# Kernel tuning notes

Measured on AMD Instinct MI355X. Metric: run time of the kernel, lower is better.

## Reference

```python
import jax, jax.numpy as jnp
import numpy as np

B, L, D, N_HEADS = 4, 8192, 1024, 16
HD = D // N_HEADS
MASK_NEG = -1e10


def setup_inputs() -> dict:
    key = jax.random.key(0)
    ks = jax.random.split(key, 5)
    # xavier_normal std for square Dense: sqrt(2/(fan_in+fan_out))
    std = (2.0 / (D + D)) ** 0.5
    return {
        "query": jax.random.normal(ks[0], (B, L, D), dtype=jnp.float32),
        "mask": jax.random.bernoulli(ks[1], 0.1, (B, L)),  # True = masked out
        "Wq": std * jax.random.normal(ks[2], (D, D), dtype=jnp.float32),
        "bq": jnp.zeros((D,), dtype=jnp.float32),
        "Wk": std * jax.random.normal(ks[3], (D, D), dtype=jnp.float32),
        "bk": jnp.zeros((D,), dtype=jnp.float32),
        "Wv": std * jax.random.normal(ks[4], (D, D), dtype=jnp.float32),
        "bv": jnp.zeros((D,), dtype=jnp.float32),
    }


def reference(query, mask, Wq, bq, Wk, bk, Wv, bv):
    # Self-attention: key = value = query (original falls back when key/value are None)
    q = query @ Wq + bq  # [B, L, D]
    k = query @ Wk + bk
    v = query @ Wv + bv
    # split heads: b l (n h) -> b l n h
    qs = q.reshape(B, L, N_HEADS, HD)
    ks_ = k.reshape(B, L, N_HEADS, HD)
    vs = v.reshape(B, L, N_HEADS, HD)
    m = mask[:, :, None, None]  # [B, L, 1, 1], broadcast over heads & dims
    K = jnp.where(m, MASK_NEG, ks_)
    V = jnp.where(m, 0.0, vs)
    # elu kernel feature map: phi(x) = elu(x) + 1 (elu(-1e10)+1 -> 0 for masked keys)
    phiK = jax.nn.elu(K) + 1.0
    phiQ = jax.nn.elu(qs) + 1.0
    # per-head kv summary: [B, N, HD_k, HD_v]
    kv = jnp.einsum('blnk,blnv->bnkv', phiK, V)
    # FAITHFUL to original einsum 'blk,bkv->blk': sums kv over v, elementwise with phiQ
    kv_sum = kv.sum(-1)  # [B, N, HD]
    out = phiQ * kv_sum[:, None, :, :]  # [B, L, N, HD]
    # combine heads: b l n h -> b l (n h)
    return out.reshape(B, L, D)
```

## Files before the change

kernel.cpp:

```cpp
#include <hip/hip_runtime.h>

typedef unsigned short u16;
typedef unsigned int u32;
typedef __attribute__((ext_vector_type(8))) short s16x8;
typedef __attribute__((ext_vector_type(4))) float f32x4;

#define GAS __attribute__((address_space(1)))
#define LAS __attribute__((address_space(3)))

#define BB 4
#define LL 8192
#define DD 1024
#define NH 16
#define HD 64
#define MROWS (BB * LL)
#define NWBT 2064

__device__ __forceinline__ u16 f2bf(float f) {
  u32 u = __builtin_bit_cast(u32, f);
  u32 r = (u + 0x7FFFu + ((u >> 16) & 1u)) >> 16;
  return (u16)r;
}
__device__ __forceinline__ float bf2f(u32 lo) {
  return __builtin_bit_cast(float, lo << 16);
}

__device__ __forceinline__ void async16(const void* g, void* l) {
  __builtin_amdgcn_global_load_lds((const GAS u32*)g, (LAS u32*)l, 16, 0, 0);
}

__device__ __forceinline__ bool get_mask(const void* mp, int row, int mode) {
  if (mode == 2) return ((const unsigned char*)mp)[row] != 0;
  if (mode == 1) return ((const float*)mp)[row] != 0.f;
  return ((const int*)mp)[row] != 0;
}

__global__ void build_wbt(const float* __restrict__ Wq, const float* __restrict__ Wk,
                          u16* __restrict__ WbT) {
  __shared__ float t[32][33];
  const int n0 = blockIdx.x * 32;
  const int k0 = blockIdx.y * 32;
  const float* W = (n0 >> 10) == 0 ? Wq : Wk;
  const int nloc = n0 & 1023;
  const int tx = threadIdx.x, ty = threadIdx.y;
#pragma unroll
  for (int j = 0; j < 32; j += 8)
    t[ty + j][tx] = W[(size_t)(k0 + ty + j) * DD + nloc + tx];
  __syncthreads();
#pragma unroll
  for (int j = 0; j < 32; j += 8)
    WbT[(size_t)(n0 + ty + j) * DD + k0 + tx] = f2bf(t[tx][ty + j]);
}

__global__ void build_aux(const float* __restrict__ Wv, const float* __restrict__ bq,
                          const float* __restrict__ bk, const float* __restrict__ bv,
                          const u32* __restrict__ m,
                          u16* __restrict__ WbT, float* __restrict__ bcat,
                          int* __restrict__ flag) {
  const int blk = blockIdx.x;
  const int tid = threadIdx.x;
  if (blk < 64) {
    int i = blk * 256 + tid;
    int k = i >> 4, h = i & 15;
    float s = 0.f;
    const float* p = Wv + (size_t)k * DD + h * HD;
#pragma unroll 8
    for (int j = 0; j < 64; ++j) s += p[j];
    WbT[(size_t)(2048 + h) * DD + k] = f2bf(s);
  } else if (blk < 73) {
    int i = (blk - 64) * 256 + tid;
    if (i < 1024) bcat[i] = bq[i];
    else if (i < 2048) bcat[i] = bk[i - 1024];
    else if (i < 2064) {
      float s = 0.f;
      const float* p = bv + (i - 2048) * HD;
#pragma unroll 8
      for (int j = 0; j < 64; ++j) s += p[j];
      bcat[i] = s;
    }
  } else {
    int i = (blk - 73) * 256 + tid;
    u32 v = m[i];
    int f = 0;
    if (v == 0x3F800000u) f = 1;
    else if (v > 1u) f = 2;
    if (f) atomicMax(flag, f);
  }
}

__global__ __launch_bounds__(256) void prep_q(
    const float* __restrict__ query, const u16* __restrict__ WbT,
    const float* __restrict__ bcat, const void* __restrict__ maskp,
    const int* __restrict__ mmode,
    u16* __restrict__ qb, float* __restrict__ sV) {
  __shared__ u16 ldsW[16 * 1024];
  __shared__ u16 ldsA[64 * 64];
  const int tid = threadIdx.x;
  const int lane = tid & 63;
  const int w = tid >> 6;
  const int l15 = lane & 15, l16 = lane >> 4;
  const int row0 = blockIdx.x * 64;

#pragma unroll
  for (int j = 0; j < 8; ++j) {
    int idx = tid + j * 256;
    int h = idx >> 7, c = idx & 127;
    s16x8 v = *(const s16x8*)(WbT + (size_t)(2048 + h) * DD + c * 8);
    *(s16x8*)(ldsW + h * 1024 + (c ^ (h & 7)) * 8) = v;
  }

  f32x4 acc = {};
  for (int k0 = 0; k0 < DD; k0 += 64) {
    __syncthreads();
#pragma unroll
    for (int j = 0; j < 2; ++j) {
      int li = tid + j * 256;
      int row = li >> 3, slot = li & 7;
      int seg = slot ^ (row & 7);
      const float* gp = query + (size_t)(row0 + row) * DD + k0 + seg * 8;
      float4 v0 = *(const float4*)gp;
      float4 v1 = *(const float4*)(gp + 4);
      s16x8 o;
      o[0] = (short)f2bf(v0.x); o[1] = (short)f2bf(v0.y);
      o[2] = (short)f2bf(v0.z); o[3] = (short)f2bf(v0.w);
      o[4] = (short)f2bf(v1.x); o[5] = (short)f2bf(v1.y);
      o[6] = (short)f2bf(v1.z); o[7] = (short)f2bf(v1.w);
      *(s16x8*)(qb + (size_t)(row0 + row) * DD + k0 + seg * 8) = o;
      *(s16x8*)(ldsA + row * 64 + slot * 8) = o;
    }
    __syncthreads();
#pragma unroll
    for (int kk = 0; kk < 2; ++kk) {
      const int segk = kk * 4 + l16;
      const int r = w * 16 + l15;
      s16x8 af = *(const s16x8*)(ldsA + r * 64 + ((segk ^ (r & 7))) * 8);
      const int cc = (k0 >> 3) + segk;
      s16x8 bfr = *(const s16x8*)(ldsW + l15 * 1024 + ((cc ^ (l15 & 7))) * 8);
      acc = __builtin_amdgcn_mfma_f32_16x16x32_bf16(af, bfr, acc, 0, 0, 0);
    }
  }

  const int mode = *mmode;
#pragma unroll
  for (int r = 0; r < 4; ++r) {
    const int row = row0 + w * 16 + l16 * 4 + r;
    const bool msk = get_mask(maskp, row, mode);
    float v = acc[r] + bcat[2048 + l15];
    sV[(size_t)row * NH + l15] = msk ? 0.f : v;
  }
}

#define BUFSZ 8192
#define UOFF(buf, mat, ks) (((((buf)*2 + (mat))*2 + (ks))) * BUFSZ)

__global__ __launch_bounds__(512, 2) void gemm_qkv(
    const u16* __restrict__ qb, const u16* __restrict__ WbT,
    const float* __restrict__ bcat, const void* __restrict__ maskp,
    const int* __restrict__ mmode,
    const float* __restrict__ sV, float* __restrict__ kv,
    float* __restrict__ out, int phase) {
  __shared__ __align__(16) u16 lds[65536];
  const int tid = threadIdx.x;
  const int lane = tid & 63;
  const int w = tid >> 6;
  const int wm = w & 1, wn = w >> 1;
  const int l15 = lane & 15, l16 = lane >> 4;

  const int bid = blockIdx.x;
  const int swz = (bid & 7) * 64 + (bid >> 3);
  const int mt = swz >> 2;
  const int nt = swz & 3;
  const int row0 = mt * 256;
  const int col0 = (phase ? 1024 : 0) + nt * 256;

  f32x4 acc[8][4] = {};

#define STAGE(buf, mat, ks, kt) do {                                        \
    const u16* gb_ = (mat) ? (WbT + (size_t)col0 * DD)                      \
                           : (qb + (size_t)row0 * DD);                      \
    const int kt_ = (kt) & 15;                                              \
    _Pragma("unroll")                                                       \
    for (int j_ = 0; j_ < 2; ++j_) {                                        \
      int li_ = tid + j_ * 512;                                             \
      int row_ = li_ >> 2, slot_ = li_ & 3;                                 \
      int c_ = slot_ ^ ((row_ >> 1) & 3);                                   \
      async16(gb_ + (size_t)row_ * DD + kt_ * 64 + (ks) * 32 + c_ * 8,      \
              lds + UOFF(buf, mat, ks) + li_ * 8);                          \
    }                                                                       \
  } while (0)

#define LDA(buf, ks, a) do {                                                \
    _Pragma("unroll")                                                       \
    for (int mi_ = 0; mi_ < 8; ++mi_) {                                     \
      int r_ = wm * 128 + mi_ * 16 + l15;                                   \
      a[mi_] = *(const s16x8*)(lds + UOFF(buf, 0, ks) + r_ * 32 +           \
                               ((l16 ^ ((r_ >> 1) & 3)) * 8));              \
    }                                                                       \
  } while (0)

#define LDB2(buf, ks, nb, b) do {                                           \
    _Pragma("unroll")                                                       \
    for (int q_ = 0; q_ < 2; ++q_) {                                        \
      int r_ = wn * 64 + ((nb)*2 + q_) * 16 + l15;                          \
      b[q_] = *(const s16x8*)(lds + UOFF(buf, 1, ks) + r_ * 32 +            \
                              ((l16 ^ ((r_ >> 1) & 3)) * 8));               \
    }                                                                       \
  } while (0)

#define MM(a, b, nb) do {                                                   \
    __builtin_amdgcn_s_setprio(1);                                          \
    _Pragma("unroll")                                                       \
    for (int mi_ = 0; mi_ < 8; ++mi_) {                                     \
      acc[mi_][(nb)*2] = __builtin_amdgcn_mfma_f32_16x16x32_bf16(           \
          a[mi_], b[0], acc[mi_][(nb)*2], 0, 0, 0);                         \
      acc[mi_][(nb)*2 + 1] = __builtin_amdgcn_mfma_f32_16x16x32_bf16(       \
          a[mi_], b[1], acc[mi_][(nb)*2 + 1], 0, 0, 0);                     \
    }                                                                       \
    __builtin_amdgcn_s_setprio(0);                                          \
  } while (0)

#define BAR() __builtin_amdgcn_s_barrier()
#define VMW6() asm volatile("s_waitcnt vmcnt(6)" ::: "memory")

  STAGE(0, 0, 0, 0); STAGE(0, 1, 0, 0); STAGE(0, 0, 1, 0); STAGE(0, 1, 1, 0);
  STAGE(1, 0, 0, 1); STAGE(1, 1, 0, 1); STAGE(1, 0, 1, 1);
  VMW6();
  BAR();

  for (int t = 0; t < 16; t += 2) {
    s16x8 a[8], b[2];
    LDA(0, 0, a); LDB2(0, 0, 0, b);
    STAGE(1, 1, 1, t + 1);
    BAR(); MM(a, b, 0); BAR();
    LDB2(0, 0, 1, b);
    STAGE(0, 0, 0, t + 2);
    BAR(); MM(a, b, 1); BAR();
    LDA(0, 1, a); LDB2(0, 1, 0, b);
    STAGE(0, 1, 0, t + 2);
    BAR(); MM(a, b, 0); BAR();
    LDB2(0, 1, 1, b);
    STAGE(0, 0, 1, t + 2);
    BAR(); MM(a, b, 1); VMW6(); BAR();
    LDA(1, 0, a); LDB2(1, 0, 0, b);
    STAGE(0, 1, 1, t + 2);
    BAR(); MM(a, b, 0); BAR();
    LDB2(1, 0, 1, b);
    STAGE(1, 0, 0, t + 3);
    BAR(); MM(a, b, 1); BAR();
    LDA(1, 1, a); LDB2(1, 1, 0, b);
    STAGE(1, 1, 0, t + 3);
    BAR(); MM(a, b, 0); BAR();
    LDB2(1, 1, 1, b);
    STAGE(1, 0, 1, t + 3);
    BAR(); MM(a, b, 1); VMW6(); BAR();
  }

  const int mode = *mmode;
  const int lanec = lane & 15, laneq = lane >> 4;
  const int wcol0 = col0 + wn * 64;
  const int b_ = row0 >> 13;

  if (phase == 1) {
    const int n = (wcol0 - 1024) >> 6;
    float pc[4] = {0.f, 0.f, 0.f, 0.f};
#pragma unroll
    for (int mi = 0; mi < 8; ++mi) {
#pragma unroll
      for (int r = 0; r < 4; ++r) {
        const int row = row0 + wm * 128 + mi * 16 + laneq * 4 + r;
        const bool msk = get_mask(maskp, row, mode);
        if (!msk) {
          const float sv = sV[(size_t)row * NH + n];
#pragma unroll
          for (int ni = 0; ni < 4; ++ni) {
            const int col = wcol0 + ni * 16 + lanec;
            float v = acc[mi][ni][r] + bcat[col];
            float phi = v > 0.f ? v + 1.f : __expf(v);
            pc[ni] += phi * sv;
          }
        }
      }
    }
#pragma unroll
    for (int ni = 0; ni < 4; ++ni) {
      pc[ni] += __shfl_xor(pc[ni], 16);
      pc[ni] += __shfl_xor(pc[ni], 32);
    }
    if (laneq == 0) {
#pragma unroll
      for (int ni = 0; ni < 4; ++ni) {
        const int colk = wcol0 - 1024 + ni * 16 + lanec;
        atomicAdd(&kv[b_ * DD + colk], pc[ni]);
      }
    }
  } else {
    float kvv[4];
#pragma unroll
    for (int ni = 0; ni < 4; ++ni)
      kvv[ni] = kv[b_ * DD + wcol0 + ni * 16 + lanec];
#pragma unroll
    for (int mi = 0; mi < 8; ++mi) {
#pragma unroll
      for (int r = 0; r < 4; ++r) {
        const int row = row0 + wm * 128 + mi * 16 + laneq * 4 + r;
#pragma unroll
        for (int ni = 0; ni < 4; ++ni) {
          const int col = wcol0 + ni * 16 + lanec;
          float v = acc[mi][ni][r] + bcat[col];
          float phi = v > 0.f ? v + 1.f : __expf(v);
          out[(size_t)row * DD + col] = phi * kvv[ni];
        }
      }
    }
  }
}

extern "C" void kernel_launch(void* const* d_in, const int* in_sizes, int n_in,
                              void* d_out, int out_size, void* d_ws, size_t ws_size,
                              hipStream_t stream) {
  const float* query = (const float*)d_in[0];
  const void* maskp = d_in[1];
  const float* Wq = (const float*)d_in[2];
  const float* bq = (const float*)d_in[3];
  const float* Wk = (const float*)d_in[4];
  const float* bk = (const float*)d_in[5];
  const float* Wv = (const float*)d_in[6];
  const float* bv = (const float*)d_in[7];
  float* out = (float*)d_out;

  char* ws = (char*)d_ws;
  u16* qb = (u16*)ws;            ws += (size_t)MROWS * DD * 2;
  u16* WbT = (u16*)ws;           ws += (size_t)NWBT * DD * 2;
  float* sV = (float*)ws;        ws += (size_t)MROWS * NH * 4;
  float* bcat = (float*)ws;      ws += (size_t)NWBT * 4;
  float* kv = (float*)ws;        ws += (size_t)BB * DD * 4;
  int* mflag = (int*)ws;         ws += 256;

  hipMemsetAsync(kv, 0, (size_t)BB * DD * 4 + 256, stream);

  build_wbt<<<dim3(2048 / 32, DD / 32), dim3(32, 8), 0, stream>>>(Wq, Wk, WbT);
  build_aux<<<105, 256, 0, stream>>>(Wv, bq, bk, bv, (const u32*)maskp, WbT, bcat, mflag);
  prep_q<<<MROWS / 64, 256, 0, stream>>>(query, WbT, bcat, maskp, mflag, qb, sV);
  gemm_qkv<<<512, 512, 0, stream>>>(qb, WbT, bcat, maskp, mflag, sV, kv, out, 1);
  gemm_qkv<<<512, 512, 0, stream>>>(qb, WbT, bcat, maskp, mflag, sV, kv, out, 0);
}
```

Before: 418.2 us.

## Load prep_q operands straight into registers and split K across wave pairs

The prep_q kernel no longer stages the 16-row WbT slice and the query tile through LDS with per-iteration barriers. Each wave now loads fp32 query rows and weight fragments directly into registers in MFMA fragment layout, converts them to bf16, stores the bf16 copy, and issues MFMAs. The K dimension is split between two waves whose partial sums are combined through a small shared buffer, and the grid doubles to 32 rows per block. This removes the LDS staging and the synchronisation overhead, at the cost of higher register pressure and redundant global loads of the weight slice across waves.

```diff
diff --git a/kernel.cpp b/kernel.cpp
--- a/kernel.cpp
+++ b/kernel.cpp
@@ -93,60 +93,58 @@
     const float* __restrict__ bcat, const void* __restrict__ maskp,
     const int* __restrict__ mmode,
     u16* __restrict__ qb, float* __restrict__ sV) {
-  __shared__ u16 ldsW[16 * 1024];
-  __shared__ u16 ldsA[64 * 64];
+  __shared__ float sVp[2][16][16];
   const int tid = threadIdx.x;
   const int lane = tid & 63;
   const int w = tid >> 6;
+  const int wl = w >> 1;
+  const int ks = w & 1;
   const int l15 = lane & 15, l16 = lane >> 4;
-  const int row0 = blockIdx.x * 64;
-
-#pragma unroll
-  for (int j = 0; j < 8; ++j) {
-    int idx = tid + j * 256;
-    int h = idx >> 7, c = idx & 127;
-    s16x8 v = *(const s16x8*)(WbT + (size_t)(2048 + h) * DD + c * 8);
-    *(s16x8*)(ldsW + h * 1024 + (c ^ (h & 7)) * 8) = v;
-  }
+  const int row0 = blockIdx.x * 32 + wl * 16;
+  const int arow = row0 + l15;
+
+  const float* qrow = query + (size_t)arow * DD + ks * 512 + l16 * 8;
+  u16* qbrow = qb + (size_t)arow * DD + ks * 512 + l16 * 8;
+  const u16* wrow = WbT + (size_t)(2048 + l15) * DD + ks * 512 + l16 * 8;
 
   f32x4 acc = {};
-  for (int k0 = 0; k0 < DD; k0 += 64) {
-    __syncthreads();
-#pragma unroll
-    for (int j = 0; j < 2; ++j) {
-      int li = tid + j * 256;
-      int row = li >> 3, slot = li & 7;
-      int seg = slot ^ (row & 7);
-      const float* gp = query + (size_t)(row0 + row) * DD + k0 + seg * 8;
-      float4 v0 = *(const float4*)gp;
-      float4 v1 = *(const float4*)(gp + 4);
+#pragma unroll
+  for (int mac = 0; mac < 2; ++mac) {
+    float4 qv[16];
+    s16x8 wv[8];
+#pragma unroll
+    for (int s = 0; s < 8; ++s) {
+      const int off = mac * 256 + s * 32;
+      qv[s * 2] = *(const float4*)(qrow + off);
+      qv[s * 2 + 1] = *(const float4*)(qrow + off + 4);
+      wv[s] = *(const s16x8*)(wrow + off);
+    }
+#pragma unroll
+    for (int s = 0; s < 8; ++s) {
       s16x8 o;
-      o[0] = (short)f2bf(v0.x); o[1] = (short)f2bf(v0.y);
-      o[2] = (short)f2bf(v0.z); o[3] = (short)f2bf(v0.w);
-      o[4] = (short)f2bf(v1.x); o[5] = (short)f2bf(v1.y);
-      o[6] = (short)f2bf(v1.z); o[7] = (short)f2bf(v1.w);
-      *(s16x8*)(qb + (size_t)(row0 + row) * DD + k0 + seg * 8) = o;
-      *(s16x8*)(ldsA + row * 64 + slot * 8) = o;
-    }
-    __syncthreads();
-#pragma unroll
-    for (int kk = 0; kk < 2; ++kk) {
-      const int segk = kk * 4 + l16;
-      const int r = w * 16 + l15;
-      s16x8 af = *(const s16x8*)(ldsA + r * 64 + ((segk ^ (r & 7))) * 8);
-      const int cc = (k0 >> 3) + segk;
-      s16x8 bfr = *(const s16x8*)(ldsW + l15 * 1024 + ((cc ^ (l15 & 7))) * 8);
-      acc = __builtin_amdgcn_mfma_f32_16x16x32_bf16(af, bfr, acc, 0, 0, 0);
-    }
-  }
-
-  const int mode = *mmode;
-#pragma unroll
-  for (int r = 0; r < 4; ++r) {
-    const int row = row0 + w * 16 + l16 * 4 + r;
-    const bool msk = get_mask(maskp, row, mode);
-    float v = acc[r] + bcat[2048 + l15];
-    sV[(size_t)row * NH + l15] = msk ? 0.f : v;
+      o[0] = (short)f2bf(qv[s * 2].x);     o[1] = (short)f2bf(qv[s * 2].y);
+      o[2] = (short)f2bf(qv[s * 2].z);     o[3] = (short)f2bf(qv[s * 2].w);
+      o[4] = (short)f2bf(qv[s * 2 + 1].x); o[5] = (short)f2bf(qv[s * 2 + 1].y);
+      o[6] = (short)f2bf(qv[s * 2 + 1].z); o[7] = (short)f2bf(qv[s * 2 + 1].w);
+      *(s16x8*)(qbrow + mac * 256 + s * 32) = o;
+      acc = __builtin_amdgcn_mfma_f32_16x16x32_bf16(o, wv[s], acc, 0, 0, 0);
+    }
+  }
+
+  if (ks == 1) {
+#pragma unroll
+    for (int r = 0; r < 4; ++r) sVp[wl][l16 * 4 + r][l15] = acc[r];
+  }
+  __syncthreads();
+  if (ks == 0) {
+    const int mode = *mmode;
+#pragma unroll
+    for (int r = 0; r < 4; ++r) {
+      const int row = row0 + l16 * 4 + r;
+      const bool msk = get_mask(maskp, row, mode);
+      float v = acc[r] + sVp[wl][l16 * 4 + r][l15] + bcat[2048 + l15];
+      sV[(size_t)row * NH + l15] = msk ? 0.f : v;
+    }
   }
 }
 
@@ -340,7 +338,7 @@
 
   build_wbt<<<dim3(2048 / 32, DD / 32), dim3(32, 8), 0, stream>>>(Wq, Wk, WbT);
   build_aux<<<105, 256, 0, stream>>>(Wv, bq, bk, bv, (const u32*)maskp, WbT, bcat, mflag);
-  prep_q<<<MROWS / 64, 256, 0, stream>>>(query, WbT, bcat, maskp, mflag, qb, sV);
+  prep_q<<<MROWS / 32, 256, 0, stream>>>(query, WbT, bcat, maskp, mflag, qb, sV);
   gemm_qkv<<<512, 512, 0, stream>>>(qb, WbT, bcat, maskp, mflag, sV, kv, out, 1);
   gemm_qkv<<<512, 512, 0, stream>>>(qb, WbT, bcat, maskp, mflag, sV, kv, out, 0);
 }
```

After: 412.1 us. Within noise of the previous version (-1.5%).
